# Kernel optimization log

Measured on AMD Instinct MI355X. Metric: run time of the kernel, lower is better.

## Reference

```python
import jax, jax.numpy as jnp
import numpy as np

L = 28; D = 1024; HQ = 16; HKV = 8; HD = 128; G = HQ // HKV
FF = 3072; VOCAB = 151936; THETA = 1000000.0; EPS = 1e-6
B = 2; PAST = 1024
SCALE = HD ** -0.5


def _rmsnorm(x, w):
    v = jnp.mean(jnp.square(x), axis=-1, keepdims=True)
    return x * jax.lax.rsqrt(v + EPS) * w


def _rotate_half(x):
    x1, x2 = jnp.split(x, 2, axis=-1)
    return jnp.concatenate([-x2, x1], axis=-1)


def setup_inputs() -> dict:
    key = jax.random.key(0)
    ks = jax.random.split(key, 12)
    s = 0.02
    return {
        "input_embeds": jax.random.normal(ks[0], (B, 1, D), jnp.float32),
        "position_ids": jax.random.randint(ks[1], (B, 1), 0, PAST).astype(jnp.int32),
        "past_keys": jax.random.normal(ks[2], (L, B, HKV, PAST, HD), jnp.float32),
        "past_values": jax.random.normal(ks[3], (L, B, HKV, PAST, HD), jnp.float32),
        "Wq": s * jax.random.normal(ks[4], (L, D, HQ * HD), jnp.float32),
        "Wk": s * jax.random.normal(ks[5], (L, D, HKV * HD), jnp.float32),
        "Wv": s * jax.random.normal(ks[6], (L, D, HKV * HD), jnp.float32),
        "Wo": s * jax.random.normal(ks[7], (L, HQ * HD, D), jnp.float32),
        "Wg": s * jax.random.normal(ks[8], (L, D, FF), jnp.float32),
        "Wu": s * jax.random.normal(ks[9], (L, D, FF), jnp.float32),
        "Wd": s * jax.random.normal(ks[10], (L, FF, D), jnp.float32),
        "ln1_w": jnp.ones((L, D), jnp.float32),
        "ln2_w": jnp.ones((L, D), jnp.float32),
        "qn_w": jnp.ones((L, HD), jnp.float32),
        "kn_w": jnp.ones((L, HD), jnp.float32),
        "final_norm_w": jnp.ones((D,), jnp.float32),
        "lm_head_w": s * jax.random.normal(ks[11], (D, VOCAB), jnp.float32),
    }


def reference(input_embeds, position_ids, past_keys, past_values,
              Wq, Wk, Wv, Wo, Wg, Wu, Wd,
              ln1_w, ln2_w, qn_w, kn_w, final_norm_w, lm_head_w):
    # Rotary embeddings for the single new position.
    pos = position_ids.astype(jnp.float32)                      # [B,1]
    inv_freq = 1.0 / (THETA ** (jnp.arange(0, HD, 2, dtype=jnp.float32) / HD))
    freqs = pos[..., None] * inv_freq                           # [B,1,HD/2]
    emb = jnp.concatenate([freqs, freqs], axis=-1)              # [B,1,HD]
    cos = jnp.cos(emb)[:, None, :, :]                           # [B,1,1,HD] (head bcast)
    sin = jnp.sin(emb)[:, None, :, :]

    def layer(h, xs):
        wq, wk, wv, wo, wg, wu, wd, l1, l2, qw, kw, pk, pv = xs
        n = _rmsnorm(h, l1)                                     # [B,1,D]
        q = _rmsnorm((n @ wq).reshape(B, 1, HQ, HD), qw).transpose(0, 2, 1, 3)   # [B,HQ,1,HD]
        k = _rmsnorm((n @ wk).reshape(B, 1, HKV, HD), kw).transpose(0, 2, 1, 3)  # [B,HKV,1,HD]
        v = (n @ wv).reshape(B, 1, HKV, HD).transpose(0, 2, 1, 3)
        q = q * cos + _rotate_half(q) * sin
        k = k * cos + _rotate_half(k) * sin
        K = jnp.concatenate([pk, k], axis=2)                    # [B,HKV,PAST+1,HD]
        V = jnp.concatenate([pv, v], axis=2)
        # GQA without materializing repeated KV: q heads grouped kv-major,
        # matching torch _repeat_kv head ordering (head = kv*G + g).
        qg = q[:, :, 0, :].reshape(B, HKV, G, HD)
        scores = jnp.einsum('bkgd,bksd->bkgs', qg, K) * SCALE
        w = jax.nn.softmax(scores.astype(jnp.float32), axis=-1).astype(q.dtype)
        o = jnp.einsum('bkgs,bksd->bkgd', w, V).reshape(B, 1, HQ * HD)
        h = h + o @ wo
        m = _rmsnorm(h, l2)
        h = h + (jax.nn.silu(m @ wg) * (m @ wu)) @ wd           # SwiGLU MLP
        return h, (K, V)

    xs = (Wq, Wk, Wv, Wo, Wg, Wu, Wd, ln1_w, ln2_w, qn_w, kn_w, past_keys, past_values)
    h, (present_keys, present_values) = jax.lax.scan(layer, input_embeds, xs)
    logits = _rmsnorm(h, final_norm_w) @ lm_head_w              # [B,1,VOCAB]
    return logits, present_keys, present_values
```

## Files before the change

### kernel.cpp

```cpp
#include <hip/hip_runtime.h>
#include <math.h>

#define NL 28
#define DIM 1024
#define NHQ 16
#define NHKV 8
#define HDIM 128
#define NG 2
#define NFF 3072
#define NVOCAB 151936
#define NB 2
#define NPAST 1024
#define NPTOT 1025
#define EPSF 1e-6f
#define QKSCALE 0.08838834764831845f
#define LOGTHETA 13.815510557964274f

#define SQKV 8
#define SCH 32
#define NCOPY 128

#define OFF_N1   0
#define OFF_H    2048
#define OFF_H1   4096
#define OFF_QKV  8192
#define OFF_AM   73728
#define OFF_AL   74752
#define OFF_AO   75776
#define OFF_WO   206848
#define OFF_G    223232
#define OFF_U    272384
#define OFF_WD   321536

#define PK_OFF ((size_t)NB*NVOCAB)
#define PV_OFF (PK_OFF + (size_t)NL*NB*NHKV*NPTOT*HDIM)
#define PK4 (PK_OFF/4)
#define PV4 (PV_OFF/4)

__device__ __forceinline__ float wave_red_sum(float v) {
  #pragma unroll
  for (int off = 32; off > 0; off >>= 1) v += __shfl_xor(v, off);
  return v;
}

__global__ __launch_bounds__(256) void k0_init(const float* __restrict__ embeds,
    const float* __restrict__ ln1, float* __restrict__ ws)
{
  int tid = threadIdx.x;
  int lane = tid & 63, w = tid >> 6;
  __shared__ float wr[8];
  int d = tid*4;
  float4 v0 = *(const float4*)(embeds + d);
  float4 v1 = *(const float4*)(embeds + DIM + d);
  float4 lw = *(const float4*)(ln1 + d);
  *(float4*)(ws + OFF_H + d) = v0;
  *(float4*)(ws + OFF_H + DIM + d) = v1;
  float s0 = wave_red_sum(v0.x*v0.x + v0.y*v0.y + v0.z*v0.z + v0.w*v0.w);
  float s1 = wave_red_sum(v1.x*v1.x + v1.y*v1.y + v1.z*v1.z + v1.w*v1.w);
  if (lane == 0) { wr[w] = s0; wr[4+w] = s1; }
  __syncthreads();
  float r0 = rsqrtf((wr[0]+wr[1]+wr[2]+wr[3])/DIM + EPSF);
  float r1 = rsqrtf((wr[4]+wr[5]+wr[6]+wr[7])/DIM + EPSF);
  float4 n0 = make_float4(v0.x*r0*lw.x, v0.y*r0*lw.y, v0.z*r0*lw.z, v0.w*r0*lw.w);
  float4 n1 = make_float4(v1.x*r1*lw.x, v1.y*r1*lw.y, v1.z*r1*lw.z, v1.w*r1*lw.w);
  *(float4*)(ws + OFF_N1 + d) = n0;
  *(float4*)(ws + OFF_N1 + DIM + d) = n1;
}

__global__ __launch_bounds__(256) void k1_qkv(
    const float* __restrict__ Wq_, const float* __restrict__ Wk_,
    const float* __restrict__ Wv_, const float* __restrict__ ln1,
    const float* __restrict__ pastK, const float* __restrict__ pastV,
    float* __restrict__ out, float* __restrict__ ws, int l)
{
  int bid = blockIdx.x;
  int tid = threadIdx.x;
  if (bid >= 512) {
    int cb = bid - 512;
    const float4* pk4 = (const float4*)pastK;
    const float4* pv4 = (const float4*)pastV;
    float4* o4 = (float4*)out;
    #pragma unroll
    for (int t = 0; t < 16; t++) {
      size_t idx = (size_t)(t*NCOPY + cb)*256 + tid;
      size_t pair = idx >> 15, j = idx & 32767;
      size_t sbase = ((size_t)l*16 + pair)*32768 + j;
      size_t dbase = ((size_t)l*16 + pair)*32800 + j;
      o4[PK4 + dbase] = pk4[sbase];
      o4[PV4 + dbase] = pv4[sbase];
    }
    return;
  }
  int bx = bid & 63, by = bid >> 6;
  int lane = tid & 63, w = tid >> 6;
  __shared__ __align__(16) float sh[NB][128];
  __shared__ __align__(16) float red[256*9];
  __shared__ float wr[8];

  int ct = tid & 15, rs = tid >> 4;
  int colg = bx*64 + ct*4;
  const float* W; int O; int wcol;
  if (bx < 32)      { W = Wq_; O = 2048; wcol = colg; }
  else if (bx < 48) { W = Wk_; O = 1024; wcol = colg - 2048; }
  else              { W = Wv_; O = 1024; wcol = colg - 3072; }
  int r0 = rs*8;
  const float* Wp = W + (size_t)l*DIM*O + (size_t)(by*128 + r0)*O + wcol;
  float4 wb[8];

  if (l == 0) {
    int b = tid >> 7, r = tid & 127;
    float nv = ws[OFF_N1 + b*DIM + by*128 + r];
    __builtin_amdgcn_sched_barrier(0);
    #pragma unroll
    for (int i = 0; i < 8; i++) wb[i] = *(const float4*)(Wp + (size_t)i*O);
    sh[b][r] = nv;
    __syncthreads();
  } else {
    int d = tid*4;
    float4 a0 = *(const float4*)(ws + OFF_H1 + d);
    float4 a1 = *(const float4*)(ws + OFF_H1 + DIM + d);
    #pragma unroll
    for (int s = 0; s < 8; s++) {
      float4 p0 = *(const float4*)(ws + OFF_WD + (s*NB + 0)*DIM + d);
      float4 p1 = *(const float4*)(ws + OFF_WD + (s*NB + 1)*DIM + d);
      a0.x += p0.x; a0.y += p0.y; a0.z += p0.z; a0.w += p0.w;
      a1.x += p1.x; a1.y += p1.y; a1.z += p1.z; a1.w += p1.w;
    }
    float4 lw = *(const float4*)(ln1 + (size_t)l*DIM + d);
    __builtin_amdgcn_sched_barrier(0);
    #pragma unroll
    for (int i = 0; i < 8; i++) wb[i] = *(const float4*)(Wp + (size_t)i*O);
    if (bx == 0 && by == 0) {
      *(float4*)(ws + OFF_H + d) = a0;
      *(float4*)(ws + OFF_H + DIM + d) = a1;
    }
    float s0 = wave_red_sum(a0.x*a0.x + a0.y*a0.y + a0.z*a0.z + a0.w*a0.w);
    float s1 = wave_red_sum(a1.x*a1.x + a1.y*a1.y + a1.z*a1.z + a1.w*a1.w);
    if (lane == 0) { wr[w] = s0; wr[4+w] = s1; }
    __syncthreads();
    float rq0 = rsqrtf((wr[0]+wr[1]+wr[2]+wr[3])/DIM + EPSF);
    float rq1 = rsqrtf((wr[4]+wr[5]+wr[6]+wr[7])/DIM + EPSF);
    int r = d - by*128;
    if (r >= 0 && r < 128) {
      sh[0][r] = a0.x*rq0*lw.x; sh[0][r+1] = a0.y*rq0*lw.y;
      sh[0][r+2] = a0.z*rq0*lw.z; sh[0][r+3] = a0.w*rq0*lw.w;
      sh[1][r] = a1.x*rq1*lw.x; sh[1][r+1] = a1.y*rq1*lw.y;
      sh[1][r+2] = a1.z*rq1*lw.z; sh[1][r+3] = a1.w*rq1*lw.w;
    }
    __syncthreads();
  }

  float a[2][4] = {};
  #pragma unroll
  for (int i = 0; i < 8; i++) {
    float x0 = sh[0][r0+i], x1 = sh[1][r0+i];
    a[0][0] += x0*wb[i].x; a[0][1] += x0*wb[i].y; a[0][2] += x0*wb[i].z; a[0][3] += x0*wb[i].w;
    a[1][0] += x1*wb[i].x; a[1][1] += x1*wb[i].y; a[1][2] += x1*wb[i].z; a[1][3] += x1*wb[i].w;
  }
  float* rp = red + tid*9;
  #pragma unroll
  for (int e = 0; e < 4; e++) { rp[e] = a[0][e]; rp[4+e] = a[1][e]; }
  __syncthreads();
  if (tid < 16) {
    float o[8] = {};
    #pragma unroll
    for (int j = 0; j < 16; j++) {
      const float* q = red + (size_t)(j*16 + tid)*9;
      #pragma unroll
      for (int e = 0; e < 8; e++) o[e] += q[e];
    }
    int cg = bx*64 + tid*4;
    #pragma unroll
    for (int e = 0; e < 4; e++) {
      ws[OFF_QKV + (by*NB + 0)*4096 + cg + e] = o[e];
      ws[OFF_QKV + (by*NB + 1)*4096 + cg + e] = o[4+e];
    }
  }
}

__global__ __launch_bounds__(256) void k2_attn(
    const float* __restrict__ pastK, const float* __restrict__ pastV,
    const int* __restrict__ posids, const float* __restrict__ qnw,
    const float* __restrict__ knw, float* __restrict__ out,
    float* __restrict__ ws, int l)
{
  int c = blockIdx.x, kv = blockIdx.y, b = blockIdx.z;
  int tid = threadIdx.x;
  int lane = tid & 63, w = tid >> 6;
  int g = tid >> 7, o = tid & 127;
  __shared__ __align__(16) float qf[NG][HDIM];
  __shared__ __align__(16) float kf[HDIM];
  __shared__ __align__(16) float vf[HDIM];
  __shared__ __align__(16) float pre[NG][HDIM];
  __shared__ __align__(16) float kpre[HDIM];
  __shared__ __align__(16) float po[8][NG][HDIM];
  __shared__ float wr[8];
  __shared__ float pm[8][NG], pl[8][NG];

  int hq = kv*NG + g;
  float qp = 0.f, kp = 0.f;
  #pragma unroll
  for (int s = 0; s < SQKV; s++) qp += ws[OFF_QKV + (s*NB + b)*4096 + hq*HDIM + o];
  int kvslot = g ? 3072 : 2048;
  #pragma unroll
  for (int s = 0; s < SQKV; s++) kp += ws[OFF_QKV + (s*NB + b)*4096 + kvslot + kv*HDIM + o];
  float qw_ = qnw[l*HDIM + o];
  float kw_ = knw[l*HDIM + o];
  float pos = (float)posids[b];
  __builtin_amdgcn_sched_barrier(0);

  int grp = tid >> 5, q = tid & 31;
  int p0 = c*32;
  size_t pastb4 = ((((size_t)l*NB + b)*NHKV + kv)*NPAST)*(HDIM/4);
  size_t presbase = ((((size_t)l*NB + b)*NHKV + kv)*NPTOT)*HDIM;
  const float4* pk4 = (const float4*)pastK;
  const float4* pv4 = (const float4*)pastV;
  float4 kk[4], vv[4];
  #pragma unroll
  for (int i = 0; i < 4; i++) {
    size_t p = p0 + grp + i*8;
    kk[i] = pk4[pastb4 + p*(HDIM/4) + q];
    vv[i] = pv4[pastb4 + p*(HDIM/4) + q];
  }
  __builtin_amdgcn_sched_barrier(0);

  float sq = wave_red_sum(qp*qp);
  float sk = wave_red_sum(kp*kp);
  if (lane == 0) { wr[w] = sq; wr[4+w] = sk; }
  __syncthreads();
  float qr = rsqrtf((wr[g<<1] + wr[(g<<1)+1])/HDIM + EPSF);
  float kr = rsqrtf((wr[4] + wr[5])/HDIM + EPSF);
  float qn = qp*qr*qw_;
  pre[g][o] = qn;
  if (g == 0) kpre[o] = kp*kr*kw_;
  else vf[o] = kp;
  __syncthreads();
  float ang = pos * expf(-(2.0f*(float)(o & 63)/(float)HDIM)*LOGTHETA);
  float sn, cs;
  sincosf(ang, &sn, &cs);
  {
    float rotq = (o < 64) ? -pre[g][o+64] : pre[g][o-64];
    qf[g][o] = qn*cs + rotq*sn;
    if (g == 0) {
      float kx = kpre[o];
      float rotk = (o < 64) ? -kpre[o+64] : kpre[o-64];
      kf[o] = kx*cs + rotk*sn;
    }
  }
  __syncthreads();

  float4 q0 = *(const float4*)&qf[0][q*4];
  float4 q1 = *(const float4*)&qf[1][q*4];
  float sc0[4], sc1[4];
  #pragma unroll
  for (int i = 0; i < 4; i++) {
    float d0 = q0.x*kk[i].x + q0.y*kk[i].y + q0.z*kk[i].z + q0.w*kk[i].w;
    float d1 = q1.x*kk[i].x + q1.y*kk[i].y + q1.z*kk[i].z + q1.w*kk[i].w;
    #pragma unroll
    for (int off = 16; off > 0; off >>= 1) {
      d0 += __shfl_xor(d0, off);
      d1 += __shfl_xor(d1, off);
    }
    sc0[i] = d0*QKSCALE; sc1[i] = d1*QKSCALE;
  }
  float xs0 = -1e30f, xs1 = -1e30f;
  float4 xv = make_float4(0.f, 0.f, 0.f, 0.f);
  if (c == SCH-1 && grp == 0) {
    float4 kX = *(const float4*)&kf[q*4];
    xv = *(const float4*)&vf[q*4];
    *(float4*)(out + PK_OFF + presbase + (size_t)NPAST*HDIM + q*4) = kX;
    *(float4*)(out + PV_OFF + presbase + (size_t)NPAST*HDIM + q*4) = xv;
    float d0 = q0.x*kX.x + q0.y*kX.y + q0.z*kX.z + q0.w*kX.w;
    float d1 = q1.x*kX.x + q1.y*kX.y + q1.z*kX.z + q1.w*kX.w;
    #pragma unroll
    for (int off = 16; off > 0; off >>= 1) {
      d0 += __shfl_xor(d0, off);
      d1 += __shfl_xor(d1, off);
    }
    xs0 = d0*QKSCALE; xs1 = d1*QKSCALE;
  }
  float m0 = fmaxf(fmaxf(sc0[0], sc0[1]), fmaxf(sc0[2], sc0[3]));
  float m1 = fmaxf(fmaxf(sc1[0], sc1[1]), fmaxf(sc1[2], sc1[3]));
  m0 = fmaxf(m0, xs0); m1 = fmaxf(m1, xs1);
  if (q == 0) { pm[grp][0] = m0; pm[grp][1] = m1; }
  __syncthreads();
  float M0 = -1e30f, M1 = -1e30f;
  #pragma unroll
  for (int j = 0; j < 8; j++) { M0 = fmaxf(M0, pm[j][0]); M1 = fmaxf(M1, pm[j][1]); }
  float l0 = 0.f, l1 = 0.f;
  float4 o0 = {0,0,0,0}, o1 = {0,0,0,0};
  #pragma unroll
  for (int j = 0; j < 4; j++) {
    float w0 = __expf(sc0[j] - M0), w1 = __expf(sc1[j] - M1);
    l0 += w0; l1 += w1;
    o0.x += w0*vv[j].x; o0.y += w0*vv[j].y; o0.z += w0*vv[j].z; o0.w += w0*vv[j].w;
    o1.x += w1*vv[j].x; o1.y += w1*vv[j].y; o1.z += w1*vv[j].z; o1.w += w1*vv[j].w;
  }
  {
    float w0 = __expf(xs0 - M0), w1 = __expf(xs1 - M1);
    l0 += w0; l1 += w1;
    o0.x += w0*xv.x; o0.y += w0*xv.y; o0.z += w0*xv.z; o0.w += w0*xv.w;
    o1.x += w1*xv.x; o1.y += w1*xv.y; o1.z += w1*xv.z; o1.w += w1*xv.w;
  }
  if (q == 0) { pl[grp][0] = l0; pl[grp][1] = l1; }
  *(float4*)&po[grp][0][q*4] = o0;
  *(float4*)&po[grp][1][q*4] = o1;
  __syncthreads();
  {
    int head = tid >> 7, dd = tid & 127;
    float acc = 0.f;
    #pragma unroll
    for (int j = 0; j < 8; j++) acc += po[j][head][dd];
    int base = ((b*NHKV + kv)*NG + head)*SCH + c;
    ws[OFF_AO + (size_t)base*HDIM + dd] = acc;
    if (dd == 0) {
      float ll = 0.f;
      #pragma unroll
      for (int j = 0; j < 8; j++) ll += pl[j][head];
      ws[OFF_AM + base] = (head ? M1 : M0);
      ws[OFF_AL + base] = ll;
    }
  }
}

__global__ __launch_bounds__(256) void k3_wo(const float* __restrict__ Wo_,
    float* __restrict__ ws, int l)
{
  int bx = blockIdx.x, by = blockIdx.y;
  int tid = threadIdx.x;
  __shared__ __align__(16) float x[NB][256];
  __shared__ float wf[NB][2][SCH];
  __shared__ float invL[NB][2];
  __shared__ __align__(16) float red[256*9];

  if (tid < 128) {
    int b = tid >> 6, hh = (tid >> 5) & 1, cc = tid & 31;
    int hb = b*16 + by*2 + hh;
    float m  = ws[OFF_AM + hb*SCH + cc];
    float ll = ws[OFF_AL + hb*SCH + cc];
    float M = m;
    #pragma unroll
    for (int off = 16; off > 0; off >>= 1) M = fmaxf(M, __shfl_xor(M, off));
    float f = __expf(m - M);
    float Ls = ll*f;
    #pragma unroll
    for (int off = 16; off > 0; off >>= 1) Ls += __shfl_xor(Ls, off);
    wf[b][hh][cc] = f;
    if (cc == 0) invL[b][hh] = 1.0f/Ls;
  }
  __builtin_amdgcn_sched_barrier(0);

  int ct = tid & 7, rs = tid >> 3;
  int col = bx*32 + ct*4;
  int r0 = rs*8;
  const float* Wp = Wo_ + (size_t)l*(NHQ*HDIM)*DIM + (size_t)(by*256 + r0)*DIM + col;
  float4 wb[8];
  #pragma unroll
  for (int i = 0; i < 8; i++) wb[i] = *(const float4*)(Wp + (size_t)i*DIM);
  __syncthreads();

  for (int e = tid; e < 512; e += 256) {
    int b = e >> 8, rr = e & 255, hh = rr >> 7, dd = rr & 127;
    int hb = b*16 + by*2 + hh;
    const float* op = ws + OFF_AO + (size_t)(hb*SCH)*HDIM + dd;
    float acc = 0.f;
    #pragma unroll
    for (int cc = 0; cc < SCH; cc++) acc += op[(size_t)cc*HDIM]*wf[b][hh][cc];
    x[b][rr] = acc*invL[b][hh];
  }
  __syncthreads();
  float a[2][4] = {};
  #pragma unroll
  for (int i = 0; i < 8; i++) {
    float x0 = x[0][r0+i], x1 = x[1][r0+i];
    a[0][0] += x0*wb[i].x; a[0][1] += x0*wb[i].y; a[0][2] += x0*wb[i].z; a[0][3] += x0*wb[i].w;
    a[1][0] += x1*wb[i].x; a[1][1] += x1*wb[i].y; a[1][2] += x1*wb[i].z; a[1][3] += x1*wb[i].w;
  }
  float* rp = red + tid*9;
  #pragma unroll
  for (int e = 0; e < 4; e++) { rp[e] = a[0][e]; rp[4+e] = a[1][e]; }
  __syncthreads();
  if (tid < 8) {
    float o[8] = {};
    #pragma unroll
    for (int j = 0; j < 32; j++) {
      const float* qq = red + (size_t)(j*8 + tid)*9;
      #pragma unroll
      for (int e = 0; e < 8; e++) o[e] += qq[e];
    }
    int cg = bx*32 + tid*4;
    #pragma unroll
    for (int e = 0; e < 4; e++) {
      ws[OFF_WO + (by*NB + 0)*DIM + cg + e] = o[e];
      ws[OFF_WO + (by*NB + 1)*DIM + cg + e] = o[4+e];
    }
  }
}

__global__ __launch_bounds__(256) void k4_mlp1(const float* __restrict__ Wg_,
    const float* __restrict__ Wu_, const float* __restrict__ ln2,
    float* __restrict__ ws, int l)
{
  int bx = blockIdx.x, by = blockIdx.y;
  int tid = threadIdx.x;
  int lane = tid & 63, w = tid >> 6;
  __shared__ __align__(16) float sh[NB][128];
  __shared__ __align__(16) float red[256*9];
  __shared__ float wr[8];

  int d = tid*4;
  float4 a0 = *(const float4*)(ws + OFF_H + d);
  float4 a1 = *(const float4*)(ws + OFF_H + DIM + d);
  #pragma unroll
  for (int s = 0; s < 8; s++) {
    float4 p0 = *(const float4*)(ws + OFF_WO + (s*NB + 0)*DIM + d);
    float4 p1 = *(const float4*)(ws + OFF_WO + (s*NB + 1)*DIM + d);
    a0.x += p0.x; a0.y += p0.y; a0.z += p0.z; a0.w += p0.w;
    a1.x += p1.x; a1.y += p1.y; a1.z += p1.z; a1.w += p1.w;
  }
  float4 lw = *(const float4*)(ln2 + (size_t)l*DIM + d);
  __builtin_amdgcn_sched_barrier(0);

  int ct = tid & 15, rs = tid >> 4;
  int col = bx*64 + ct*4;
  int r0 = rs*8;
  const float* Wgp = Wg_ + (size_t)l*DIM*NFF + (size_t)(by*128 + r0)*NFF + col;
  const float* Wup = Wu_ + (size_t)l*DIM*NFF + (size_t)(by*128 + r0)*NFF + col;
  float4 wg[8], wu[8];
  #pragma unroll
  for (int i = 0; i < 8; i++) {
    wg[i] = *(const float4*)(Wgp + (size_t)i*NFF);
    wu[i] = *(const float4*)(Wup + (size_t)i*NFF);
  }

  if (bx == 0 && by == 0) {
    *(float4*)(ws + OFF_H1 + d) = a0;
    *(float4*)(ws + OFF_H1 + DIM + d) = a1;
  }
  float s0 = wave_red_sum(a0.x*a0.x + a0.y*a0.y + a0.z*a0.z + a0.w*a0.w);
  float s1 = wave_red_sum(a1.x*a1.x + a1.y*a1.y + a1.z*a1.z + a1.w*a1.w);
  if (lane == 0) { wr[w] = s0; wr[4+w] = s1; }
  __syncthreads();
  float rq0 = rsqrtf((wr[0]+wr[1]+wr[2]+wr[3])/DIM + EPSF);
  float rq1 = rsqrtf((wr[4]+wr[5]+wr[6]+wr[7])/DIM + EPSF);
  int r = d - by*128;
  if (r >= 0 && r < 128) {
    sh[0][r] = a0.x*rq0*lw.x; sh[0][r+1] = a0.y*rq0*lw.y;
    sh[0][r+2] = a0.z*rq0*lw.z; sh[0][r+3] = a0.w*rq0*lw.w;
    sh[1][r] = a1.x*rq1*lw.x; sh[1][r+1] = a1.y*rq1*lw.y;
    sh[1][r+2] = a1.z*rq1*lw.z; sh[1][r+3] = a1.w*rq1*lw.w;
  }
  __syncthreads();

  float ag[2][4] = {}, au[2][4] = {};
  #pragma unroll
  for (int i = 0; i < 8; i++) {
    float x0 = sh[0][r0+i], x1 = sh[1][r0+i];
    ag[0][0] += x0*wg[i].x; ag[0][1] += x0*wg[i].y; ag[0][2] += x0*wg[i].z; ag[0][3] += x0*wg[i].w;
    ag[1][0] += x1*wg[i].x; ag[1][1] += x1*wg[i].y; ag[1][2] += x1*wg[i].z; ag[1][3] += x1*wg[i].w;
    au[0][0] += x0*wu[i].x; au[0][1] += x0*wu[i].y; au[0][2] += x0*wu[i].z; au[0][3] += x0*wu[i].w;
    au[1][0] += x1*wu[i].x; au[1][1] += x1*wu[i].y; au[1][2] += x1*wu[i].z; au[1][3] += x1*wu[i].w;
  }
  float* rp = red + tid*9;
  #pragma unroll
  for (int e = 0; e < 4; e++) { rp[e] = ag[0][e]; rp[4+e] = ag[1][e]; }
  __syncthreads();
  if (tid < 16) {
    float o[8] = {};
    #pragma unroll
    for (int j = 0; j < 16; j++) {
      const float* qq = red + (size_t)(j*16 + tid)*9;
      #pragma unroll
      for (int e = 0; e < 8; e++) o[e] += qq[e];
    }
    int cg = bx*64 + tid*4;
    #pragma unroll
    for (int e = 0; e < 4; e++) {
      ws[OFF_G + (by*NB + 0)*NFF + cg + e] = o[e];
      ws[OFF_G + (by*NB + 1)*NFF + cg + e] = o[4+e];
    }
  }
  __syncthreads();
  #pragma unroll
  for (int e = 0; e < 4; e++) { rp[e] = au[0][e]; rp[4+e] = au[1][e]; }
  __syncthreads();
  if (tid < 16) {
    float o[8] = {};
    #pragma unroll
    for (int j = 0; j < 16; j++) {
      const float* qq = red + (size_t)(j*16 + tid)*9;
      #pragma unroll
      for (int e = 0; e < 8; e++) o[e] += qq[e];
    }
    int cg = bx*64 + tid*4;
    #pragma unroll
    for (int e = 0; e < 4; e++) {
      ws[OFF_U + (by*NB + 0)*NFF + cg + e] = o[e];
      ws[OFF_U + (by*NB + 1)*NFF + cg + e] = o[4+e];
    }
  }
}

__global__ __launch_bounds__(256) void k5_mlp2(const float* __restrict__ Wd_,
    float* __restrict__ ws, int l)
{
  int bx = blockIdx.x, by = blockIdx.y;
  int tid = threadIdx.x;
  __shared__ __align__(16) float act[NB][384];
  __shared__ __align__(16) float red[256*9];

  float4 gacc = {0,0,0,0}, uacc = {0,0,0,0};
  int pb = 0, pf4 = 0;
  if (tid < 192) {
    pb = tid / 96; pf4 = tid % 96;
    int f4 = (by*384)/4 + pf4;
    const float4* Gp = (const float4*)(ws + OFF_G);
    const float4* Up = (const float4*)(ws + OFF_U);
    #pragma unroll
    for (int s = 0; s < 8; s++) {
      float4 g4 = Gp[(size_t)(s*NB + pb)*(NFF/4) + f4];
      float4 u4 = Up[(size_t)(s*NB + pb)*(NFF/4) + f4];
      gacc.x += g4.x; gacc.y += g4.y; gacc.z += g4.z; gacc.w += g4.w;
      uacc.x += u4.x; uacc.y += u4.y; uacc.z += u4.z; uacc.w += u4.w;
    }
  }
  __builtin_amdgcn_sched_barrier(0);

  int ct = tid & 7, rs = tid >> 3;
  int col = bx*32 + ct*4;
  int r0 = rs*12;
  const float* Wp = Wd_ + (size_t)l*NFF*DIM + (size_t)(by*384 + r0)*DIM + col;
  float4 wb[12];
  #pragma unroll
  for (int i = 0; i < 12; i++) wb[i] = *(const float4*)(Wp + (size_t)i*DIM);

  if (tid < 192) {
    float4 r;
    r.x = (gacc.x / (1.0f + __expf(-gacc.x)))*uacc.x;
    r.y = (gacc.y / (1.0f + __expf(-gacc.y)))*uacc.y;
    r.z = (gacc.z / (1.0f + __expf(-gacc.z)))*uacc.z;
    r.w = (gacc.w / (1.0f + __expf(-gacc.w)))*uacc.w;
    *(float4*)&act[pb][pf4*4] = r;
  }
  __syncthreads();

  float a[2][4] = {};
  #pragma unroll
  for (int i = 0; i < 12; i++) {
    float x0 = act[0][r0+i], x1 = act[1][r0+i];
    a[0][0] += x0*wb[i].x; a[0][1] += x0*wb[i].y; a[0][2] += x0*wb[i].z; a[0][3] += x0*wb[i].w;
    a[1][0] += x1*wb[i].x; a[1][1] += x1*wb[i].y; a[1][2] += x1*wb[i].z; a[1][3] += x1*wb[i].w;
  }
  float* rp = red + tid*9;
  #pragma unroll
  for (int e = 0; e < 4; e++) { rp[e] = a[0][e]; rp[4+e] = a[1][e]; }
  __syncthreads();
  if (tid < 8) {
    float o[8] = {};
    #pragma unroll
    for (int j = 0; j < 32; j++) {
      const float* qq = red + (size_t)(j*8 + tid)*9;
      #pragma unroll
      for (int e = 0; e < 8; e++) o[e] += qq[e];
    }
    int cg = bx*32 + tid*4;
    #pragma unroll
    for (int e = 0; e < 4; e++) {
      ws[OFF_WD + (by*NB + 0)*DIM + cg + e] = o[e];
      ws[OFF_WD + (by*NB + 1)*DIM + cg + e] = o[4+e];
    }
  }
}

__global__ __launch_bounds__(256) void kf_final(const float* __restrict__ fnw,
    float* __restrict__ ws)
{
  int tid = threadIdx.x;
  int lane = tid & 63, w = tid >> 6;
  __shared__ float wr[8];
  int d = tid*4;
  float4 a0 = *(const float4*)(ws + OFF_H1 + d);
  float4 a1 = *(const float4*)(ws + OFF_H1 + DIM + d);
  #pragma unroll
  for (int s = 0; s < 8; s++) {
    float4 p0 = *(const float4*)(ws + OFF_WD + (s*NB + 0)*DIM + d);
    float4 p1 = *(const float4*)(ws + OFF_WD + (s*NB + 1)*DIM + d);
    a0.x += p0.x; a0.y += p0.y; a0.z += p0.z; a0.w += p0.w;
    a1.x += p1.x; a1.y += p1.y; a1.z += p1.z; a1.w += p1.w;
  }
  float4 fw = *(const float4*)(fnw + d);
  float s0 = wave_red_sum(a0.x*a0.x + a0.y*a0.y + a0.z*a0.z + a0.w*a0.w);
  float s1 = wave_red_sum(a1.x*a1.x + a1.y*a1.y + a1.z*a1.z + a1.w*a1.w);
  if (lane == 0) { wr[w] = s0; wr[4+w] = s1; }
  __syncthreads();
  float rq0 = rsqrtf((wr[0]+wr[1]+wr[2]+wr[3])/DIM + EPSF);
  float rq1 = rsqrtf((wr[4]+wr[5]+wr[6]+wr[7])/DIM + EPSF);
  float4 n0 = make_float4(a0.x*rq0*fw.x, a0.y*rq0*fw.y, a0.z*rq0*fw.z, a0.w*rq0*fw.w);
  float4 n1 = make_float4(a1.x*rq1*fw.x, a1.y*rq1*fw.y, a1.z*rq1*fw.z, a1.w*rq1*fw.w);
  *(float4*)(ws + OFF_N1 + d) = n0;
  *(float4*)(ws + OFF_N1 + DIM + d) = n1;
}

__global__ __launch_bounds__(256) void k6_lmhead(const float* __restrict__ lmw,
    const float* __restrict__ ws, float* __restrict__ out)
{
  __shared__ __align__(16) float nf[NB*DIM];
  __shared__ __align__(16) float red[256*9];
  int tid = threadIdx.x;
  *(float4*)&nf[tid*4]        = *(const float4*)(ws + OFF_N1 + tid*4);
  *(float4*)&nf[1024 + tid*4] = *(const float4*)(ws + OFF_N1 + 1024 + tid*4);
  __syncthreads();

  int ct = tid & 15, rs = tid >> 4;
  int col = blockIdx.x*64 + ct*4;
  const float* Wp = lmw + (size_t)(rs*64)*NVOCAB + col;
  float a[2][4] = {};
  for (int t = 0; t < 8; t++) {
    float4 wb[8];
    #pragma unroll
    for (int i = 0; i < 8; i++)
      wb[i] = *(const float4*)(Wp + (size_t)(t*8 + i)*NVOCAB);
    #pragma unroll
    for (int i = 0; i < 8; i++) {
      int rr = rs*64 + t*8 + i;
      float x0 = nf[rr], x1 = nf[DIM+rr];
      a[0][0] += x0*wb[i].x; a[0][1] += x0*wb[i].y; a[0][2] += x0*wb[i].z; a[0][3] += x0*wb[i].w;
      a[1][0] += x1*wb[i].x; a[1][1] += x1*wb[i].y; a[1][2] += x1*wb[i].z; a[1][3] += x1*wb[i].w;
    }
  }
  float* rp = red + tid*9;
  #pragma unroll
  for (int e = 0; e < 4; e++) { rp[e] = a[0][e]; rp[4+e] = a[1][e]; }
  __syncthreads();
  if (tid < 16) {
    float o[8] = {};
    #pragma unroll
    for (int j = 0; j < 16; j++) {
      const float* qq = red + (size_t)(j*16 + tid)*9;
      #pragma unroll
      for (int e = 0; e < 8; e++) o[e] += qq[e];
    }
    int cg = blockIdx.x*64 + tid*4;
    #pragma unroll
    for (int e = 0; e < 4; e++) {
      out[cg + e] = o[e];
      out[NVOCAB + cg + e] = o[4+e];
    }
  }
}

extern "C" void kernel_launch(void* const* d_in, const int* in_sizes, int n_in,
                              void* d_out, int out_size, void* d_ws, size_t ws_size,
                              hipStream_t stream) {
  (void)in_sizes; (void)n_in; (void)out_size; (void)ws_size;
  const float* embeds = (const float*)d_in[0];
  const int*   posids = (const int*)d_in[1];
  const float* pastK  = (const float*)d_in[2];
  const float* pastV  = (const float*)d_in[3];
  const float* Wq     = (const float*)d_in[4];
  const float* Wk     = (const float*)d_in[5];
  const float* Wv     = (const float*)d_in[6];
  const float* Wo     = (const float*)d_in[7];
  const float* Wg     = (const float*)d_in[8];
  const float* Wu     = (const float*)d_in[9];
  const float* Wd     = (const float*)d_in[10];
  const float* ln1    = (const float*)d_in[11];
  const float* ln2    = (const float*)d_in[12];
  const float* qnw    = (const float*)d_in[13];
  const float* knw    = (const float*)d_in[14];
  const float* fnw    = (const float*)d_in[15];
  const float* lmw    = (const float*)d_in[16];
  float* out = (float*)d_out;
  float* ws  = (float*)d_ws;

  k0_init<<<1, 256, 0, stream>>>(embeds, ln1, ws);
  for (int l = 0; l < NL; l++) {
    k1_qkv <<<512 + NCOPY, 256, 0, stream>>>(Wq, Wk, Wv, ln1, pastK, pastV, out, ws, l);
    k2_attn<<<dim3(SCH, NHKV, NB), 256, 0, stream>>>(pastK, pastV, posids, qnw, knw, out, ws, l);
    k3_wo  <<<dim3(32, 8), 256, 0, stream>>>(Wo, ws, l);
    k4_mlp1<<<dim3(48, 8), 256, 0, stream>>>(Wg, Wu, ln2, ws, l);
    k5_mlp2<<<dim3(32, 8), 256, 0, stream>>>(Wd, ws, l);
  }
  kf_final<<<1, 256, 0, stream>>>(fnw, ws);
  k6_lmhead<<<NVOCAB/64, 256, 0, stream>>>(lmw, ws, out);
}
```

Before: 1.321 ms.

## Fold init into QKV kernel, double copy blocks, retile MLP1 grid

Removes the separate init kernel by having layer-0 QKV blocks load embeddings directly and compute the RMSNorm inline. Doubles the number of KV-cache copy blocks and halves each block's per-thread copy loop. Retiles the gate/up projection kernel to narrower 32-column tiles with 4 rows per thread, doubling the grid to 768 blocks. The aim is more parallelism and one fewer launch, at the cost of a longer serial reduction in the MLP1 blocks and less work per thread.

Measured after the change: 1.332 ms. No clear change (+0.8%).

```diff
diff --git a/kernel.cpp b/kernel.cpp
--- a/kernel.cpp
+++ b/kernel.cpp
@@ -18,7 +18,7 @@
 
 #define SQKV 8
 #define SCH 32
-#define NCOPY 128
+#define NCOPY 256
 
 #define OFF_N1   0
 #define OFF_H    2048
@@ -43,31 +43,8 @@
   return v;
 }
 
-__global__ __launch_bounds__(256) void k0_init(const float* __restrict__ embeds,
-    const float* __restrict__ ln1, float* __restrict__ ws)
-{
-  int tid = threadIdx.x;
-  int lane = tid & 63, w = tid >> 6;
-  __shared__ float wr[8];
-  int d = tid*4;
-  float4 v0 = *(const float4*)(embeds + d);
-  float4 v1 = *(const float4*)(embeds + DIM + d);
-  float4 lw = *(const float4*)(ln1 + d);
-  *(float4*)(ws + OFF_H + d) = v0;
-  *(float4*)(ws + OFF_H + DIM + d) = v1;
-  float s0 = wave_red_sum(v0.x*v0.x + v0.y*v0.y + v0.z*v0.z + v0.w*v0.w);
-  float s1 = wave_red_sum(v1.x*v1.x + v1.y*v1.y + v1.z*v1.z + v1.w*v1.w);
-  if (lane == 0) { wr[w] = s0; wr[4+w] = s1; }
-  __syncthreads();
-  float r0 = rsqrtf((wr[0]+wr[1]+wr[2]+wr[3])/DIM + EPSF);
-  float r1 = rsqrtf((wr[4]+wr[5]+wr[6]+wr[7])/DIM + EPSF);
-  float4 n0 = make_float4(v0.x*r0*lw.x, v0.y*r0*lw.y, v0.z*r0*lw.z, v0.w*r0*lw.w);
-  float4 n1 = make_float4(v1.x*r1*lw.x, v1.y*r1*lw.y, v1.z*r1*lw.z, v1.w*r1*lw.w);
-  *(float4*)(ws + OFF_N1 + d) = n0;
-  *(float4*)(ws + OFF_N1 + DIM + d) = n1;
-}
-
 __global__ __launch_bounds__(256) void k1_qkv(
+    const float* __restrict__ embeds,
     const float* __restrict__ Wq_, const float* __restrict__ Wk_,
     const float* __restrict__ Wv_, const float* __restrict__ ln1,
     const float* __restrict__ pastK, const float* __restrict__ pastV,
@@ -81,7 +58,7 @@
     const float4* pv4 = (const float4*)pastV;
     float4* o4 = (float4*)out;
     #pragma unroll
-    for (int t = 0; t < 16; t++) {
+    for (int t = 0; t < 8; t++) {
       size_t idx = (size_t)(t*NCOPY + cb)*256 + tid;
       size_t pair = idx >> 15, j = idx & 32767;
       size_t sbase = ((size_t)l*16 + pair)*32768 + j;
@@ -107,26 +84,23 @@
   const float* Wp = W + (size_t)l*DIM*O + (size_t)(by*128 + r0)*O + wcol;
   float4 wb[8];
 
-  if (l == 0) {
-    int b = tid >> 7, r = tid & 127;
-    float nv = ws[OFF_N1 + b*DIM + by*128 + r];
-    __builtin_amdgcn_sched_barrier(0);
-    #pragma unroll
-    for (int i = 0; i < 8; i++) wb[i] = *(const float4*)(Wp + (size_t)i*O);
-    sh[b][r] = nv;
-    __syncthreads();
-  } else {
+  {
     int d = tid*4;
-    float4 a0 = *(const float4*)(ws + OFF_H1 + d);
-    float4 a1 = *(const float4*)(ws + OFF_H1 + DIM + d);
-    #pragma unroll
-    for (int s = 0; s < 8; s++) {
-      float4 p0 = *(const float4*)(ws + OFF_WD + (s*NB + 0)*DIM + d);
-      float4 p1 = *(const float4*)(ws + OFF_WD + (s*NB + 1)*DIM + d);
-      a0.x += p0.x; a0.y += p0.y; a0.z += p0.z; a0.w += p0.w;
-      a1.x += p1.x; a1.y += p1.y; a1.z += p1.z; a1.w += p1.w;
-    }
-    float4 lw = *(const float4*)(ln1 + (size_t)l*DIM + d);
+    float4 a0, a1, lw = *(const float4*)(ln1 + (size_t)l*DIM + d);
+    if (l == 0) {
+      a0 = *(const float4*)(embeds + d);
+      a1 = *(const float4*)(embeds + DIM + d);
+    } else {
+      a0 = *(const float4*)(ws + OFF_H1 + d);
+      a1 = *(const float4*)(ws + OFF_H1 + DIM + d);
+      #pragma unroll
+      for (int s = 0; s < 8; s++) {
+        float4 p0 = *(const float4*)(ws + OFF_WD + (s*NB + 0)*DIM + d);
+        float4 p1 = *(const float4*)(ws + OFF_WD + (s*NB + 1)*DIM + d);
+        a0.x += p0.x; a0.y += p0.y; a0.z += p0.z; a0.w += p0.w;
+        a1.x += p1.x; a1.y += p1.y; a1.z += p1.z; a1.w += p1.w;
+      }
+    }
     __builtin_amdgcn_sched_barrier(0);
     #pragma unroll
     for (int i = 0; i < 8; i++) wb[i] = *(const float4*)(Wp + (size_t)i*O);
@@ -421,14 +395,14 @@
   float4 lw = *(const float4*)(ln2 + (size_t)l*DIM + d);
   __builtin_amdgcn_sched_barrier(0);
 
-  int ct = tid & 15, rs = tid >> 4;
-  int col = bx*64 + ct*4;
-  int r0 = rs*8;
+  int ct = tid & 7, rs = tid >> 3;
+  int col = bx*32 + ct*4;
+  int r0 = rs*4;
   const float* Wgp = Wg_ + (size_t)l*DIM*NFF + (size_t)(by*128 + r0)*NFF + col;
   const float* Wup = Wu_ + (size_t)l*DIM*NFF + (size_t)(by*128 + r0)*NFF + col;
-  float4 wg[8], wu[8];
-  #pragma unroll
-  for (int i = 0; i < 8; i++) {
+  float4 wg[4], wu[4];
+  #pragma unroll
+  for (int i = 0; i < 4; i++) {
     wg[i] = *(const float4*)(Wgp + (size_t)i*NFF);
     wu[i] = *(const float4*)(Wup + (size_t)i*NFF);
   }
@@ -454,7 +428,7 @@
 
   float ag[2][4] = {}, au[2][4] = {};
   #pragma unroll
-  for (int i = 0; i < 8; i++) {
+  for (int i = 0; i < 4; i++) {
     float x0 = sh[0][r0+i], x1 = sh[1][r0+i];
     ag[0][0] += x0*wg[i].x; ag[0][1] += x0*wg[i].y; ag[0][2] += x0*wg[i].z; ag[0][3] += x0*wg[i].w;
     ag[1][0] += x1*wg[i].x; ag[1][1] += x1*wg[i].y; ag[1][2] += x1*wg[i].z; ag[1][3] += x1*wg[i].w;
@@ -465,15 +439,15 @@
   #pragma unroll
   for (int e = 0; e < 4; e++) { rp[e] = ag[0][e]; rp[4+e] = ag[1][e]; }
   __syncthreads();
-  if (tid < 16) {
+  if (tid < 8) {
     float o[8] = {};
     #pragma unroll
-    for (int j = 0; j < 16; j++) {
-      const float* qq = red + (size_t)(j*16 + tid)*9;
+    for (int j = 0; j < 32; j++) {
+      const float* qq = red + (size_t)(j*8 + tid)*9;
       #pragma unroll
       for (int e = 0; e < 8; e++) o[e] += qq[e];
     }
-    int cg = bx*64 + tid*4;
+    int cg = bx*32 + tid*4;
     #pragma unroll
     for (int e = 0; e < 4; e++) {
       ws[OFF_G + (by*NB + 0)*NFF + cg + e] = o[e];
@@ -484,15 +458,15 @@
   #pragma unroll
   for (int e = 0; e < 4; e++) { rp[e] = au[0][e]; rp[4+e] = au[1][e]; }
   __syncthreads();
-  if (tid < 16) {
+  if (tid < 8) {
     float o[8] = {};
     #pragma unroll
-    for (int j = 0; j < 16; j++) {
-      const float* qq = red + (size_t)(j*16 + tid)*9;
+    for (int j = 0; j < 32; j++) {
+      const float* qq = red + (size_t)(j*8 + tid)*9;
       #pragma unroll
       for (int e = 0; e < 8; e++) o[e] += qq[e];
     }
-    int cg = bx*64 + tid*4;
+    int cg = bx*32 + tid*4;
     #pragma unroll
     for (int e = 0; e < 4; e++) {
       ws[OFF_U + (by*NB + 0)*NFF + cg + e] = o[e];
@@ -673,12 +647,11 @@
   float* out = (float*)d_out;
   float* ws  = (float*)d_ws;
 
-  k0_init<<<1, 256, 0, stream>>>(embeds, ln1, ws);
   for (int l = 0; l < NL; l++) {
-    k1_qkv <<<512 + NCOPY, 256, 0, stream>>>(Wq, Wk, Wv, ln1, pastK, pastV, out, ws, l);
+    k1_qkv <<<512 + NCOPY, 256, 0, stream>>>(embeds, Wq, Wk, Wv, ln1, pastK, pastV, out, ws, l);
     k2_attn<<<dim3(SCH, NHKV, NB), 256, 0, stream>>>(pastK, pastV, posids, qnw, knw, out, ws, l);
     k3_wo  <<<dim3(32, 8), 256, 0, stream>>>(Wo, ws, l);
-    k4_mlp1<<<dim3(48, 8), 256, 0, stream>>>(Wg, Wu, ln2, ws, l);
+    k4_mlp1<<<dim3(96, 8), 256, 0, stream>>>(Wg, Wu, ln2, ws, l);
     k5_mlp2<<<dim3(32, 8), 256, 0, stream>>>(Wd, ws, l);
   }
   kf_final<<<1, 256, 0, stream>>>(fnw, ws);
```
